# Optimization experiments

Hardware: AMD Instinct MI355X
Metric: run time of the kernel (lower is better)

The kernel has to match this reference:

```python
import jax, jax.numpy as jnp
import numpy as np

N = 256      # batch size
A = 2048     # in_features
B = 64       # out_features (discrimination features)
C = 32       # kernel dimension


def setup_inputs() -> dict:
    key = jax.random.key(0)
    kf, kT = jax.random.split(key)
    f = jax.random.normal(kf, (N, A), dtype=jnp.float32)
    T = jax.random.normal(kT, (A, B * C), dtype=jnp.float32)  # nn.Parameter, normal(0,1) init
    return {"f": f, "T": T}


def reference(f, T):
    # M: (n, B, C) kernel features per sample
    M = (f @ T).reshape(-1, B, C)
    # pairwise L1 distance over C: (n, n, B); |M_j - M_i| summed over kernel dim
    L1 = jnp.abs(M[None, :, :, :] - M[:, None, :, :]).sum(axis=3)
    # similarity c = exp(-L1), summed over the other samples (includes self term exp(0)=1,
    # matching the original torch code)
    o = jnp.exp(-L1).sum(axis=0)  # (n, B)
    return jnp.concatenate([f, o], axis=1)  # (n, A + B)
```

## Files before the change

kernel.cpp:

```cpp
#include <hip/hip_runtime.h>

#define OUTW 2112

typedef float          f32x4  __attribute__((ext_vector_type(4)));
typedef short          bf16x8 __attribute__((ext_vector_type(8)));
typedef unsigned short u16x4  __attribute__((ext_vector_type(4)));
typedef unsigned short u16x8  __attribute__((ext_vector_type(8)));

static __device__ __forceinline__ unsigned short bft(float x) {
  union { float f; unsigned int u; } v; v.f = x;
  return (unsigned short)(v.u >> 16);
}

static __device__ __forceinline__ void gload_lds16(const void* g, void* l) {
  __builtin_amdgcn_global_load_lds(
      (const __attribute__((address_space(1))) unsigned int*)g,
      (__attribute__((address_space(3))) unsigned int*)l, 16, 0, 0);
}

__global__ __launch_bounds__(256) void convert_k(const float* __restrict__ T,
                                                 const float* __restrict__ f,
                                                 unsigned short* __restrict__ Tt,
                                                 unsigned short* __restrict__ f16,
                                                 float* __restrict__ out) {
  const int bid = blockIdx.x, t = threadIdx.x;
  if (bid < 1024) {
    __shared__ alignas(16) unsigned short tile[64][72];
    const int kt = (bid >> 5) * 64, nt = (bid & 31) * 64;
    const int c16 = t & 15, r = t >> 4;
#pragma unroll
    for (int i = 0; i < 4; ++i) {
      int kr = r + 16 * i;
      f32x4 v = *(const f32x4*)(T + (kt + kr) * 2048 + nt + c16 * 4);
#pragma unroll
      for (int e = 0; e < 4; ++e) tile[c16 * 4 + e][kr] = bft(v[e]);
    }
    __syncthreads();
#pragma unroll
    for (int i = 0; i < 2; ++i) {
      int cid = t + 256 * i;
      int nl = cid >> 3, c = cid & 7;
      u16x8 v = *(const u16x8*)&tile[nl][c * 8];
      *(u16x8*)(Tt + (nt + nl) * 2048 + kt + c * 8) = v;
    }
  } else {
    const int fid = (bid - 1024) * 256 + t;
#pragma unroll
    for (int i = 0; i < 16; ++i) {
      int u = fid + 8192 * i;
      int row = u >> 9, c4 = (u & 511) * 4;
      f32x4 v = *(const f32x4*)(f + row * 2048 + c4);
      *(f32x4*)(out + row * OUTW + c4) = v;
      u16x4 h = { bft(v[0]), bft(v[1]), bft(v[2]), bft(v[3]) };
      *(u16x4*)(f16 + row * 2048 + c4) = h;
    }
  }
}

__global__ __launch_bounds__(256) void gemm_m(const unsigned short* __restrict__ f16,
                                              const unsigned short* __restrict__ Tt,
                                              float* __restrict__ M) {
  __shared__ alignas(16) unsigned char smem[4][12288];

  const int bid = blockIdx.x;
  const int m0 = (bid >> 6) * 64;
  const int n0 = (bid & 63) * 32;
  const int t = threadIdx.x, lane = t & 63, w = t >> 6;
  const int wr = w >> 1, wc = w & 1;

  const int lr = lane >> 3;
  const int lc = (lane & 7) ^ lr;
  const unsigned short* aSrc0 = f16 + (m0 + w * 8 + lr) * 2048 + lc * 8;
  const unsigned short* aSrc1 = aSrc0 + 32 * 2048;
  const unsigned short* bSrc  = Tt  + (n0 + w * 8 + lr) * 2048 + lc * 8;

#define STAGE(ss) {                                              \
    const int koff = (ss) * 64;                                  \
    unsigned char* base = smem[(ss) & 3];                        \
    gload_lds16(aSrc0 + koff, base + w * 1024);                  \
    gload_lds16(aSrc1 + koff, base + 4096 + w * 1024);           \
    gload_lds16(bSrc  + koff, base + 8192 + w * 1024);           \
  }

  f32x4 acc0 = {0.f, 0.f, 0.f, 0.f};
  f32x4 acc1 = {0.f, 0.f, 0.f, 0.f};

  STAGE(0) STAGE(1) STAGE(2)

  const int r0 = wr * 32 + (lane & 15);
  const int nl = wc * 16 + (lane & 15);
  const int hi = lane >> 4;
  const int swA = r0 & 7, swB = nl & 7;

#pragma unroll
  for (int step = 0; step < 32; ++step) {
    if (step == 31)      { asm volatile("s_waitcnt vmcnt(0)" ::: "memory"); }
    else if (step == 30) { asm volatile("s_waitcnt vmcnt(3)" ::: "memory"); }
    else                 { asm volatile("s_waitcnt vmcnt(6)" ::: "memory"); }
    __builtin_amdgcn_s_barrier();
    asm volatile("" ::: "memory");

    const unsigned char* Ab = smem[step & 3];
#pragma unroll
    for (int kk = 0; kk < 2; ++kk) {
      const int cg = kk * 4 + hi;
      bf16x8 a0 = *(const bf16x8*)(Ab + r0 * 128        + ((cg ^ swA) << 4));
      bf16x8 a1 = *(const bf16x8*)(Ab + (r0 + 16) * 128 + ((cg ^ swA) << 4));
      bf16x8 bb = *(const bf16x8*)(Ab + 8192 + nl * 128 + ((cg ^ swB) << 4));
      acc0 = __builtin_amdgcn_mfma_f32_16x16x32_bf16(a0, bb, acc0, 0, 0, 0);
      acc1 = __builtin_amdgcn_mfma_f32_16x16x32_bf16(a1, bb, acc1, 0, 0, 0);
    }
    if (step < 29) STAGE(step + 3)
  }
#undef STAGE

  const int col = n0 + wc * 16 + (lane & 15);
  const int rb  = m0 + wr * 32 + (hi << 2);
#pragma unroll
  for (int r = 0; r < 4; ++r) {
    M[(rb + r) * 2048 + col]      = acc0[r];
    M[(rb + 16 + r) * 2048 + col] = acc1[r];
  }
}

__global__ __launch_bounds__(256) void pairwise(const float* __restrict__ Mws,
                                                float* __restrict__ out) {
  __shared__ alignas(16) float Ml[32][260];
  __shared__ float red[32][33];

  const int b  = blockIdx.x;
  const int js = blockIdx.y;
  const int t  = threadIdx.x;

#pragma unroll
  for (int it = 0; it < 8; ++it) {
    int i = it * 32 + (t >> 3), c0 = (t & 7) * 4;
    f32x4 v = *(const f32x4*)(Mws + i * 2048 + b * 32 + c0);
    Ml[c0 + 0][i] = v[0]; Ml[c0 + 1][i] = v[1];
    Ml[c0 + 2][i] = v[2]; Ml[c0 + 3][i] = v[3];
  }
  __syncthreads();

  const int jb = t & 7, ir = t >> 3;
  const int j0 = js * 32 + jb * 4;

  f32x4 mjA[16];
#pragma unroll
  for (int c = 0; c < 16; ++c) mjA[c] = *(const f32x4*)&Ml[c][j0];

  float opart[4] = {0.f, 0.f, 0.f, 0.f};

#pragma unroll
  for (int cell = 0; cell < 2; ++cell) {
    const int i0 = (ir + 32 * cell) * 4;
    float acc[4][4];
#pragma unroll
    for (int jj = 0; jj < 4; ++jj)
#pragma unroll
      for (int ii = 0; ii < 4; ++ii) acc[jj][ii] = 0.f;

#pragma unroll
    for (int c = 0; c < 16; ++c) {
      f32x4 mi = *(const f32x4*)&Ml[c][i0];
#pragma unroll
      for (int jj = 0; jj < 4; ++jj)
#pragma unroll
        for (int ii = 0; ii < 4; ++ii)
          acc[jj][ii] += fabsf(mjA[c][jj] - mi[ii]);
    }
    float mn = acc[0][0];
#pragma unroll
    for (int jj = 0; jj < 4; ++jj)
#pragma unroll
      for (int ii = 0; ii < 4; ++ii) mn = fminf(mn, acc[jj][ii]);

    if (!__all(mn > 30.0f)) {
#pragma unroll
      for (int c = 16; c < 32; ++c) {
        f32x4 mj = *(const f32x4*)&Ml[c][j0];
        f32x4 mi = *(const f32x4*)&Ml[c][i0];
#pragma unroll
        for (int jj = 0; jj < 4; ++jj)
#pragma unroll
          for (int ii = 0; ii < 4; ++ii)
            acc[jj][ii] += fabsf(mj[jj] - mi[ii]);
      }
    }
#pragma unroll
    for (int jj = 0; jj < 4; ++jj)
#pragma unroll
      for (int ii = 0; ii < 4; ++ii)
        opart[jj] += __expf(-acc[jj][ii]);
  }

#pragma unroll
  for (int jj = 0; jj < 4; ++jj) red[ir][jb * 4 + jj] = opart[jj];
  __syncthreads();
  if (t < 32) {
    float s = 0.f;
#pragma unroll
    for (int r = 0; r < 32; ++r) s += red[r][t];
    out[(js * 32 + t) * OUTW + 2048 + b] = s;
  }
}

extern "C" void kernel_launch(void* const* d_in, const int* in_sizes, int n_in,
                              void* d_out, int out_size, void* d_ws, size_t ws_size,
                              hipStream_t stream) {
  const float* f = (const float*)d_in[0];
  const float* T = (const float*)d_in[1];
  float* out = (float*)d_out;

  unsigned short* Tt  = (unsigned short*)d_ws;
  unsigned short* f16 = (unsigned short*)((char*)d_ws + 8388608);
  float*          M   = (float*)((char*)d_ws + 9437184);

  convert_k<<<1056,        256, 0, stream>>>(T, f, Tt, f16, out);
  gemm_m   <<<256,         256, 0, stream>>>(f16, Tt, M);
  pairwise <<<dim3(64, 8), 256, 0, stream>>>(M, out);
}
```

Measured before the change: 27.99 us.

## Split GEMM K dimension in two and sum partials in pairwise loader

The GEMM now splits K=2048 into two halves over 512 blocks, so more CUs get work. Each stage loads a 128-wide K slab, kept in three LDS buffers instead of four 64-wide ones, and alternating accumulators shorten the MFMA dependency chains. The two partial M results go to separate workspace slices and are added when the pairwise kernel loads them. In exchange it writes and reads twice the M traffic, and the larger LDS footprint may limit occupancy.

```diff
diff --git a/kernel.cpp b/kernel.cpp
--- a/kernel.cpp
+++ b/kernel.cpp
@@ -57,69 +57,81 @@
   }
 }
 
-__global__ __launch_bounds__(256) void gemm_m(const unsigned short* __restrict__ f16,
-                                              const unsigned short* __restrict__ Tt,
-                                              float* __restrict__ M) {
-  __shared__ alignas(16) unsigned char smem[4][12288];
+__global__ __launch_bounds__(256, 2) void gemm_m(const unsigned short* __restrict__ f16,
+                                                 const unsigned short* __restrict__ Tt,
+                                                 float* __restrict__ M) {
+  __shared__ alignas(16) unsigned char smem[3][24576];
 
   const int bid = blockIdx.x;
-  const int m0 = (bid >> 6) * 64;
-  const int n0 = (bid & 63) * 32;
+  const int ksp = bid >> 8;
+  const int rr  = bid & 255;
+  const int m0  = (rr >> 6) * 64;
+  const int n0  = (rr & 63) * 32;
   const int t = threadIdx.x, lane = t & 63, w = t >> 6;
   const int wr = w >> 1, wc = w & 1;
-
-  const int lr = lane >> 3;
-  const int lc = (lane & 7) ^ lr;
-  const unsigned short* aSrc0 = f16 + (m0 + w * 8 + lr) * 2048 + lc * 8;
-  const unsigned short* aSrc1 = aSrc0 + 32 * 2048;
-  const unsigned short* bSrc  = Tt  + (n0 + w * 8 + lr) * 2048 + lc * 8;
-
-#define STAGE(ss) {                                              \
-    const int koff = (ss) * 64;                                  \
-    unsigned char* base = smem[(ss) & 3];                        \
-    gload_lds16(aSrc0 + koff, base + w * 1024);                  \
-    gload_lds16(aSrc1 + koff, base + 4096 + w * 1024);           \
-    gload_lds16(bSrc  + koff, base + 8192 + w * 1024);           \
-  }
-
-  f32x4 acc0 = {0.f, 0.f, 0.f, 0.f};
-  f32x4 acc1 = {0.f, 0.f, 0.f, 0.f};
-
-  STAGE(0) STAGE(1) STAGE(2)
+  const int k0 = ksp * 1024;
+
+  const unsigned short* src[6];
+#pragma unroll
+  for (int i = 0; i < 6; ++i) {
+    const int j = w * 6 + i;
+    const int rowl = lane >> 4, cs = lane & 15;
+    int row; const unsigned short* base;
+    if (j < 16) { row = j * 4 + rowl;        base = f16 + (m0 + row) * 2048; }
+    else        { row = (j - 16) * 4 + rowl; base = Tt  + (n0 + row) * 2048; }
+    src[i] = base + k0 + (cs ^ (row & 7)) * 8;
+  }
+
+#define STAGE(ss) {                                                     \
+    unsigned char* bufp = smem[(ss) % 3];                               \
+    _Pragma("unroll")                                                   \
+    for (int i = 0; i < 6; ++i)                                         \
+      gload_lds16(src[i] + (ss) * 128, bufp + (w * 6 + i) * 1024);      \
+  }
+
+  f32x4 acc[2][2];
+#pragma unroll
+  for (int a = 0; a < 2; ++a)
+#pragma unroll
+    for (int b = 0; b < 2; ++b) acc[a][b] = f32x4{0.f, 0.f, 0.f, 0.f};
+
+  STAGE(0) STAGE(1)
 
   const int r0 = wr * 32 + (lane & 15);
   const int nl = wc * 16 + (lane & 15);
   const int hi = lane >> 4;
-  const int swA = r0 & 7, swB = nl & 7;
-
-#pragma unroll
-  for (int step = 0; step < 32; ++step) {
-    if (step == 31)      { asm volatile("s_waitcnt vmcnt(0)" ::: "memory"); }
-    else if (step == 30) { asm volatile("s_waitcnt vmcnt(3)" ::: "memory"); }
-    else                 { asm volatile("s_waitcnt vmcnt(6)" ::: "memory"); }
+  const int swA = (r0 & 7) << 4, swB = (nl & 7) << 4;
+
+#pragma unroll
+  for (int step = 0; step < 8; ++step) {
+    if (step == 7) { asm volatile("s_waitcnt vmcnt(0)" ::: "memory"); }
+    else           { asm volatile("s_waitcnt vmcnt(6)" ::: "memory"); }
     __builtin_amdgcn_s_barrier();
     asm volatile("" ::: "memory");
 
-    const unsigned char* Ab = smem[step & 3];
-#pragma unroll
-    for (int kk = 0; kk < 2; ++kk) {
-      const int cg = kk * 4 + hi;
-      bf16x8 a0 = *(const bf16x8*)(Ab + r0 * 128        + ((cg ^ swA) << 4));
-      bf16x8 a1 = *(const bf16x8*)(Ab + (r0 + 16) * 128 + ((cg ^ swA) << 4));
-      bf16x8 bb = *(const bf16x8*)(Ab + 8192 + nl * 128 + ((cg ^ swB) << 4));
-      acc0 = __builtin_amdgcn_mfma_f32_16x16x32_bf16(a0, bb, acc0, 0, 0, 0);
-      acc1 = __builtin_amdgcn_mfma_f32_16x16x32_bf16(a1, bb, acc1, 0, 0, 0);
-    }
-    if (step < 29) STAGE(step + 3)
+    const unsigned char* Ab = smem[step % 3];
+#pragma unroll
+    for (int kk = 0; kk < 4; ++kk) {
+      const int cgk = (kk * 4 + hi) << 4;
+      bf16x8 a0 = *(const bf16x8*)(Ab + r0 * 256        + (cgk ^ swA));
+      bf16x8 a1 = *(const bf16x8*)(Ab + (r0 + 16) * 256 + (cgk ^ swA));
+      bf16x8 bb = *(const bf16x8*)(Ab + 16384 + nl * 256 + (cgk ^ swB));
+      acc[0][kk & 1] = __builtin_amdgcn_mfma_f32_16x16x32_bf16(a0, bb, acc[0][kk & 1], 0, 0, 0);
+      acc[1][kk & 1] = __builtin_amdgcn_mfma_f32_16x16x32_bf16(a1, bb, acc[1][kk & 1], 0, 0, 0);
+    }
+    if (step < 6) STAGE(step + 2)
   }
 #undef STAGE
 
+  float* Mp = M + ksp * (256 * 2048);
   const int col = n0 + wc * 16 + (lane & 15);
-  const int rb  = m0 + wr * 32 + (hi << 2);
+  const int rb  = m0 + wr * 32 + hi * 4;
+  f32x4 o0 = acc[0][0] + acc[0][1];
+  f32x4 o1 = acc[1][0] + acc[1][1];
 #pragma unroll
   for (int r = 0; r < 4; ++r) {
-    M[(rb + r) * 2048 + col]      = acc0[r];
-    M[(rb + 16 + r) * 2048 + col] = acc1[r];
+    Mp[(rb + r) * 2048 + col]      = o0[r];
+    Mp[(rb + 16 + r) * 2048 + col] = o1[r];
   }
 }
 
@@ -135,7 +147,9 @@
 #pragma unroll
   for (int it = 0; it < 8; ++it) {
     int i = it * 32 + (t >> 3), c0 = (t & 7) * 4;
-    f32x4 v = *(const f32x4*)(Mws + i * 2048 + b * 32 + c0);
+    f32x4 v0 = *(const f32x4*)(Mws + i * 2048 + b * 32 + c0);
+    f32x4 v1 = *(const f32x4*)(Mws + 524288 + i * 2048 + b * 32 + c0);
+    f32x4 v = v0 + v1;
     Ml[c0 + 0][i] = v[0]; Ml[c0 + 1][i] = v[1];
     Ml[c0 + 2][i] = v[2]; Ml[c0 + 3][i] = v[3];
   }
@@ -216,6 +230,6 @@
   float*          M   = (float*)((char*)d_ws + 9437184);
 
   convert_k<<<1056,        256, 0, stream>>>(T, f, Tt, f16, out);
-  gemm_m   <<<256,         256, 0, stream>>>(f16, Tt, M);
+  gemm_m   <<<512,         256, 0, stream>>>(f16, Tt, M);
   pairwise <<<dim3(64, 8), 256, 0, stream>>>(M, out);
 }
```

Result: no change. 27.75 us (-0.8%).
